# Performance work log

Measured on AMD Instinct MI355X. Metric: run time of the kernel, lower is better.

Reference implementation:

```python
import jax, jax.numpy as jnp
import numpy as np


def setup_inputs() -> dict:
    key = jax.random.key(0)
    ks = jax.random.split(key, 11)
    B, E, R, D = 2048, 20000, 500, 256
    inp = {
        "h": jax.random.uniform(ks[0], (B, E), dtype=jnp.float32),
        "t": jax.random.uniform(ks[1], (B, E), dtype=jnp.float32),
        "r": jax.random.uniform(ks[2], (B, R), dtype=jnp.float32),
        "W_er": jax.random.normal(ks[3], (D, E), dtype=jnp.float32) * 0.02,
        "W_ei": jax.random.normal(ks[4], (D, E), dtype=jnp.float32) * 0.02,
        "W_ej": jax.random.normal(ks[5], (D, E), dtype=jnp.float32) * 0.02,
        "W_ek": jax.random.normal(ks[6], (D, E), dtype=jnp.float32) * 0.02,
        "W_rr": jax.random.normal(ks[7], (D, R), dtype=jnp.float32) * 0.02,
        "W_ri": jax.random.normal(ks[8], (D, R), dtype=jnp.float32) * 0.02,
        "W_rj": jax.random.normal(ks[9], (D, R), dtype=jnp.float32) * 0.02,
        "W_rk": jax.random.normal(ks[10], (D, R), dtype=jnp.float32) * 0.02,
    }
    return inp


def reference(h, t, r, W_er, W_ei, W_ej, W_ek, W_rr, W_ri, W_rj, W_rk):
    # entity / relation projections (nn.Linear, no bias): x @ W^T -> [B, D]
    H_r, H_i, H_j, H_k = h @ W_er.T, h @ W_ei.T, h @ W_ej.T, h @ W_ek.T
    T_r, T_i, T_j, T_k = t @ W_er.T, t @ W_ei.T, t @ W_ej.T, t @ W_ek.T
    R_r, R_i, R_j, R_k = r @ W_rr.T, r @ W_ri.T, r @ W_rj.T, r @ W_rk.T

    # hypercomplex norm per row: sqrt(|R_r|^2 + |R_i|^2 + |R_j|^2 + |R_k|^2) -> [B,1]
    norm = jnp.sqrt(
        jnp.sum(R_r * R_r + R_i * R_i + R_j * R_j + R_k * R_k, axis=1, keepdims=True)
    )
    R_r, R_i, R_j, R_k = norm * R_r, norm * R_i, norm * R_j, norm * R_k

    # Hamilton product H (x) R
    Q_r = H_r * R_r - H_i * R_i - H_j * R_j - H_k * R_k
    Q_i = H_r * R_i + H_i * R_r + H_j * R_k - H_k * R_j
    Q_j = H_r * R_j - H_i * R_k + H_j * R_r + H_k * R_i
    Q_k = H_r * R_k + H_i * R_j - H_j * R_i + H_k * R_r

    # diag(Q @ T^T) == rowwise dot sum(Q*T, axis=1) -- O(B*d) form of the anti-pattern
    score = jnp.sum(Q_r * T_r + Q_i * T_i + Q_j * T_j + Q_k * T_k, axis=1, keepdims=True)
    return jax.nn.sigmoid(score)
```

## Files before the change

kernel.cpp:

```cpp
#include <hip/hip_runtime.h>


using bf16x8 = __attribute__((ext_vector_type(8))) short;
using f32x4  = __attribute__((ext_vector_type(4))) float;
using f32x16 = __attribute__((ext_vector_type(16))) float;

#define DEVINL static __device__ __forceinline__

DEVINL void split2(float x0, float x1, unsigned& h, unsigned& l) {
  unsigned u0 = __float_as_uint(x0), u1 = __float_as_uint(x1);
  unsigned h0 = u0 & 0xFFFF0000u, h1 = u1 & 0xFFFF0000u;
  h = (u0 >> 16) | h1;
  float r0 = x0 - __uint_as_float(h0);
  float r1 = x1 - __uint_as_float(h1);
  l = (__float_as_uint(r0) >> 16) | (__float_as_uint(r1) & 0xFFFF0000u);
}

DEVINL void gload16(const void* g, void* l) {
  __builtin_amdgcn_global_load_lds(
      (const __attribute__((address_space(1))) unsigned*)g,
      (__attribute__((address_space(3))) unsigned*)l, 16, 0, 0);
}

__global__ void convert_img(const float* __restrict__ src0,
                            const float* __restrict__ src1, int rows0,
                            int srcK, char* __restrict__ dst, int ktiles)
{
  const int kt = blockIdx.x, rt = blockIdx.y;
  const int m  = threadIdx.x;
  const int row = rt * 256 + m;
  const float* srow = (row < rows0) ? (src0 + (size_t)row * srcK)
                                    : (src1 + (size_t)(row - rows0) * srcK);
  char* base = dst + ((size_t)rt * ktiles + kt) * 32768
             + (m >> 5) * 2048 + (m & 31) * 16;
#pragma unroll
  for (int oct = 0; oct < 4; ++oct) {
    int k0 = kt * 32 + oct * 8;
    float x[8];
    if (k0 + 8 <= srcK) {
      float4 v0 = *(const float4*)(srow + k0);
      float4 v1 = *(const float4*)(srow + k0 + 4);
      x[0] = v0.x; x[1] = v0.y; x[2] = v0.z; x[3] = v0.w;
      x[4] = v1.x; x[5] = v1.y; x[6] = v1.z; x[7] = v1.w;
    } else {
#pragma unroll
      for (int j = 0; j < 8; ++j) x[j] = (k0 + j < srcK) ? srow[k0 + j] : 0.f;
    }
    unsigned hh[4], ll[4];
    split2(x[0], x[1], hh[0], ll[0]);
    split2(x[2], x[3], hh[1], ll[1]);
    split2(x[4], x[5], hh[2], ll[2]);
    split2(x[6], x[7], hh[3], ll[3]);
    int off = (oct >> 1) * 1024 + (oct & 1) * 512;
    *(uint4*)(base + off)         = make_uint4(hh[0], hh[1], hh[2], hh[3]);
    *(uint4*)(base + 16384 + off) = make_uint4(ll[0], ll[1], ll[2], ll[3]);
  }
}

__global__ __launch_bounds__(512, 2) void gemm_img(
    const char* __restrict__ Aimg, const char* __restrict__ Bimg, int ktiles,
    float* __restrict__ C, int MT, int NT, int KS, int swz)
{
  __shared__ __align__(16) char smem[131072];
  const int tid = threadIdx.x;
  const int bid = blockIdx.x;

  int mt, nt, ks;
  if (swz) {
    int x = bid & 7, w = bid >> 3;
    nt = w & 3;
    int g = x + (w >> 2) * 8;
    mt = g & 15; ks = g >> 4;
  } else {
    nt = bid % NT; int q = bid / NT; mt = q % MT; ks = q / MT;
  }

  const int kt0 = (ktiles * ks) / KS;
  const int kt1 = (ktiles * (ks + 1)) / KS;

  const char* Ab = Aimg + ((size_t)mt * ktiles + kt0) * 32768;
  const char* Bb = Bimg + ((size_t)nt * ktiles + kt0) * 32768;

  const int wid = tid >> 6, lane = tid & 63;
  const int wr = wid >> 2, wc = wid & 3;

  f32x16 acc[4][2];
#pragma unroll
  for (int mb = 0; mb < 4; ++mb)
#pragma unroll
    for (int nb = 0; nb < 2; ++nb)
#pragma unroll
      for (int e = 0; e < 16; ++e) acc[mb][nb][e] = 0.f;

  {
    const char* As = Ab + wid * 4096 + lane * 16;
    const char* Bs = Bb + wid * 4096 + lane * 16;
#pragma unroll
    for (int i = 0; i < 4; ++i) gload16(As + i * 1024, smem + wid * 4096 + i * 1024);
#pragma unroll
    for (int i = 0; i < 4; ++i) gload16(Bs + i * 1024, smem + 32768 + wid * 4096 + i * 1024);
  }
  asm volatile("s_waitcnt vmcnt(0)" ::: "memory");
  __builtin_amdgcn_s_barrier();

  for (int kt = kt0; kt < kt1; ++kt) {
    char* bufc = smem + (size_t)((kt - kt0) & 1) * 65536;
    char* bufn = smem + (size_t)(((kt - kt0) & 1) ^ 1) * 65536;
    const bool nx = (kt + 1 < kt1);

    if (nx) {
      const char* As = Ab + (size_t)(kt + 1 - kt0) * 32768 + wid * 4096 + lane * 16;
      const char* Bs = Bb + (size_t)(kt + 1 - kt0) * 32768 + wid * 4096 + lane * 16;
#pragma unroll
      for (int i = 0; i < 4; ++i) gload16(As + i * 1024, bufn + wid * 4096 + i * 1024);
#pragma unroll
      for (int i = 0; i < 4; ++i) gload16(Bs + i * 1024, bufn + 32768 + wid * 4096 + i * 1024);
    }

    bf16x8 bh[2][2], bl[2][2];
#pragma unroll
    for (int nb = 0; nb < 2; ++nb)
#pragma unroll
      for (int s = 0; s < 2; ++s) {
        const char* p = bufc + 32768 + (wc * 2 + nb) * 2048 + s * 1024 + lane * 16;
        bh[nb][s] = *(const bf16x8*)p;
        bl[nb][s] = *(const bf16x8*)(p + 16384);
      }

    __builtin_amdgcn_s_setprio(1);
#pragma unroll
    for (int mb = 0; mb < 4; ++mb) {
      const char* p = bufc + (wr * 4 + mb) * 2048 + lane * 16;
      bf16x8 ah0 = *(const bf16x8*)(p);
      bf16x8 al0 = *(const bf16x8*)(p + 16384);
      bf16x8 ah1 = *(const bf16x8*)(p + 1024);
      bf16x8 al1 = *(const bf16x8*)(p + 1024 + 16384);
#pragma unroll
      for (int nb = 0; nb < 2; ++nb) {
        f32x16* a = &acc[mb][nb];
        *a = __builtin_amdgcn_mfma_f32_32x32x16_bf16(ah0, bh[nb][0], *a, 0, 0, 0);
        *a = __builtin_amdgcn_mfma_f32_32x32x16_bf16(al0, bh[nb][0], *a, 0, 0, 0);
        *a = __builtin_amdgcn_mfma_f32_32x32x16_bf16(ah0, bl[nb][0], *a, 0, 0, 0);
        *a = __builtin_amdgcn_mfma_f32_32x32x16_bf16(ah1, bh[nb][1], *a, 0, 0, 0);
        *a = __builtin_amdgcn_mfma_f32_32x32x16_bf16(al1, bh[nb][1], *a, 0, 0, 0);
        *a = __builtin_amdgcn_mfma_f32_32x32x16_bf16(ah1, bl[nb][1], *a, 0, 0, 0);
      }
    }
    __builtin_amdgcn_s_setprio(0);

    asm volatile("s_waitcnt vmcnt(0)" ::: "memory");
    __builtin_amdgcn_s_barrier();
  }

  float* Cb = C + (size_t)ks * (size_t)(MT * 256) * 1024;
  const long rowbase = (long)mt * 256 + wr * 128 + 4 * (lane >> 5);
  const long colbase = (long)nt * 256 + wc * 64 + (lane & 31);
#pragma unroll
  for (int mb = 0; mb < 4; ++mb)
#pragma unroll
    for (int nb = 0; nb < 2; ++nb)
#pragma unroll
      for (int reg = 0; reg < 16; ++reg) {
        long row = rowbase + mb * 32 + (reg & 3) + 8 * (reg >> 2);
        long col = colbase + nb * 32;
        Cb[(size_t)row * 1024 + col] = acc[mb][nb][reg];
      }
}

__global__ void convert_b16(const float* __restrict__ src, int srcK,
                            char* __restrict__ dst)
{
  const int tile = blockIdx.x;
  const int wrow = threadIdx.x;
  char* base = dst + (size_t)tile * 32768;
  const float* srow = src + (size_t)wrow * srcK;
#pragma unroll
  for (int kc8 = 0; kc8 < 4; ++kc8) {
    int k0 = tile * 32 + kc8 * 8;
    float x[8];
    if (k0 + 8 <= srcK) {
      float4 v0 = *(const float4*)(srow + k0);
      float4 v1 = *(const float4*)(srow + k0 + 4);
      x[0] = v0.x; x[1] = v0.y; x[2] = v0.z; x[3] = v0.w;
      x[4] = v1.x; x[5] = v1.y; x[6] = v1.z; x[7] = v1.w;
    } else {
#pragma unroll
      for (int j = 0; j < 8; ++j) x[j] = (k0 + j < srcK) ? srow[k0 + j] : 0.f;
    }
    unsigned hh[4], ll[4];
    split2(x[0], x[1], hh[0], ll[0]);
    split2(x[2], x[3], hh[1], ll[1]);
    split2(x[4], x[5], hh[2], ll[2]);
    split2(x[6], x[7], hh[3], ll[3]);
    int lchunk = (wrow & 15) + kc8 * 16;
    int n16 = wrow >> 4;
    *(uint4*)(base + (size_t)n16 * 1024 + lchunk * 16)         = make_uint4(hh[0], hh[1], hh[2], hh[3]);
    *(uint4*)(base + 16384 + (size_t)n16 * 1024 + lchunk * 16) = make_uint4(ll[0], ll[1], ll[2], ll[3]);
  }
}

__global__ void pad_r(const float* __restrict__ src, float* __restrict__ dst)
{
  int row = blockIdx.y;
  int k = threadIdx.x * 4;
  float4 v = make_float4(0.f, 0.f, 0.f, 0.f);
  if (k + 3 < 500) v = *(const float4*)(src + (size_t)row * 500 + k);
  *(float4*)(dst + (size_t)row * 512 + k) = v;
}

__global__ __launch_bounds__(512, 2) void gemm3p(
    const float* __restrict__ A0, const float* __restrict__ A1, int mtA0, long lda,
    const char* __restrict__ Bimg, int ktilesTot,
    float* __restrict__ C, long ldc, int MT, int NT, int KS, int swz)
{
  extern __shared__ char smemd[];
  const int tid = threadIdx.x;
  const int bid = blockIdx.x;

  int mt, nt, ks;
  if (swz) {
    int x = bid & 7, w = bid >> 3;
    nt = w & 3;
    int g = x + (w >> 2) * 8;
    mt = g & 15; ks = g >> 4;
  } else {
    nt = bid % NT; int q = bid / NT; mt = q % MT; ks = q / MT;
  }

  const int kt0 = (ktilesTot * ks) / KS;
  const int kt1 = (ktilesTot * (ks + 1)) / KS;

  const float* Ablk = (mt < mtA0) ? (A0 + (size_t)mt * 256 * lda)
                                  : (A1 + (size_t)(mt - mtA0) * 256 * lda);
  const char* Bt = Bimg + ((size_t)nt * ktilesTot + kt0) * 32768;

  const int wid = tid >> 6, lane = tid & 63;
  const int wr = wid >> 2, wc = wid & 3;
  const int l15 = lane & 15, lq = lane >> 4;

  const float* aSrc = Ablk + (size_t)(wid * 32 + (lane >> 3)) * lda
                      + (size_t)kt0 * 32 + 4 * (lane & 7);

  int awoff[4];
  {
    int kg = (lane & 7) >> 1, half = lane & 1;
#pragma unroll
    for (int i = 0; i < 4; ++i) {
      int m15 = (lane >> 3) + 8 * (i & 1);
      awoff[i] = (2 * wid + (i >> 1)) * 2048 + (((m15 ^ kg) + kg * 16) << 4) + half * 8;
    }
  }
  const int aroff = (((l15 ^ lq) + lq * 16) << 4);
  const int bbase = 32768 + (wc * 4) * 1024 + lane * 16;

  f32x4 acc[8][4];
#pragma unroll
  for (int m = 0; m < 8; ++m)
#pragma unroll
    for (int j = 0; j < 4; ++j)
#pragma unroll
      for (int e = 0; e < 4; ++e) acc[m][j][e] = 0.f;

  float4 aR[4];

#define ISSUE_A(KT)                                                            \
  {                                                                            \
    const float* p_ = aSrc + (size_t)((KT) - kt0) * 32;                        \
    _Pragma("unroll")                                                          \
    for (int i = 0; i < 4; ++i) aR[i] = *(const float4*)(p_ + (size_t)(8 * i) * lda); \
  }
#define ISSUE_B(DST, KT)                                                       \
  {                                                                            \
    const char* p_ = Bt + (size_t)((KT) - kt0) * 32768 + wid * 4096 + lane * 16; \
    _Pragma("unroll")                                                          \
    for (int i = 0; i < 4; ++i)                                                \
      gload16(p_ + i * 1024, (DST) + 32768 + wid * 4096 + i * 1024);           \
  }
#define WRITE_A(DST)                                                           \
  {                                                                            \
    _Pragma("unroll")                                                          \
    for (int i = 0; i < 4; ++i) {                                              \
      unsigned h0_, l0_, h1_, l1_;                                             \
      split2(aR[i].x, aR[i].y, h0_, l0_);                                      \
      split2(aR[i].z, aR[i].w, h1_, l1_);                                      \
      *(uint2*)((DST) + awoff[i])        = make_uint2(h0_, h1_);               \
      *(uint2*)((DST) + awoff[i] + 1024) = make_uint2(l0_, l1_);               \
    }                                                                          \
  }

  ISSUE_A(kt0);
  ISSUE_B(smemd, kt0);
  WRITE_A(smemd);
  asm volatile("s_waitcnt vmcnt(0)" ::: "memory");
  asm volatile("s_waitcnt lgkmcnt(0)" ::: "memory");
  __builtin_amdgcn_s_barrier();

  for (int kt = kt0; kt < kt1; ++kt) {
    char* bufc = smemd + (size_t)((kt - kt0) & 1) * 65536;
    char* bufn = smemd + (size_t)(((kt - kt0) & 1) ^ 1) * 65536;
    const bool nx = (kt + 1 < kt1);

    if (nx) { ISSUE_A(kt + 1); ISSUE_B(bufn, kt + 1); }

    bf16x8 bh[4], bl[4];
#pragma unroll
    for (int j = 0; j < 4; ++j) {
      bh[j] = *(const bf16x8*)(bufc + bbase + j * 1024);
      bl[j] = *(const bf16x8*)(bufc + bbase + j * 1024 + 16384);
    }

    __builtin_amdgcn_s_setprio(1);
#pragma unroll
    for (int m = 0; m < 4; ++m) {
      const char* ab = bufc + (wr * 8 + m) * 2048;
      bf16x8 ah = *(const bf16x8*)(ab + aroff);
      bf16x8 al = *(const bf16x8*)(ab + aroff + 1024);
#pragma unroll
      for (int j = 0; j < 4; ++j) {
        acc[m][j] = __builtin_amdgcn_mfma_f32_16x16x32_bf16(ah, bh[j], acc[m][j], 0, 0, 0);
        acc[m][j] = __builtin_amdgcn_mfma_f32_16x16x32_bf16(al, bh[j], acc[m][j], 0, 0, 0);
        acc[m][j] = __builtin_amdgcn_mfma_f32_16x16x32_bf16(ah, bl[j], acc[m][j], 0, 0, 0);
      }
    }
    __builtin_amdgcn_s_setprio(0);

    __builtin_amdgcn_sched_barrier(0);
    if (nx) WRITE_A(bufn);

    __builtin_amdgcn_s_setprio(1);
#pragma unroll
    for (int m = 4; m < 8; ++m) {
      const char* ab = bufc + (wr * 8 + m) * 2048;
      bf16x8 ah = *(const bf16x8*)(ab + aroff);
      bf16x8 al = *(const bf16x8*)(ab + aroff + 1024);
#pragma unroll
      for (int j = 0; j < 4; ++j) {
        acc[m][j] = __builtin_amdgcn_mfma_f32_16x16x32_bf16(ah, bh[j], acc[m][j], 0, 0, 0);
        acc[m][j] = __builtin_amdgcn_mfma_f32_16x16x32_bf16(al, bh[j], acc[m][j], 0, 0, 0);
        acc[m][j] = __builtin_amdgcn_mfma_f32_16x16x32_bf16(ah, bl[j], acc[m][j], 0, 0, 0);
      }
    }
    __builtin_amdgcn_s_setprio(0);

    asm volatile("s_waitcnt vmcnt(0)" ::: "memory");
    asm volatile("s_waitcnt lgkmcnt(0)" ::: "memory");
    __builtin_amdgcn_s_barrier();
  }
#undef ISSUE_A
#undef ISSUE_B
#undef WRITE_A

  float* Cb = C + (size_t)ks * (size_t)(MT * 256) * (size_t)ldc;
  const long rowbase = (long)mt * 256 + wr * 128 + lq * 4;
  const long colbase = (long)nt * 256 + wc * 64 + l15;
#pragma unroll
  for (int m = 0; m < 8; ++m)
#pragma unroll
    for (int j = 0; j < 4; ++j)
#pragma unroll
      for (int reg = 0; reg < 4; ++reg) {
        long row = rowbase + m * 16 + reg;
        long col = colbase + j * 16;
        Cb[(size_t)row * ldc + col] = acc[m][j][reg];
      }
}

__global__ void epilogue_kernel(const float* __restrict__ C1, const float* __restrict__ C2,
                                float* __restrict__ out, int KS)
{
  const int b = blockIdx.x;
  const int d = threadIdx.x;
  const size_t SZ = 4096ull * 1024ull;

  float Hq[4], Tq[4], Rq[4];
#pragma unroll
  for (int q = 0; q < 4; ++q) {
    float hv = 0.f, tv = 0.f;
    for (int ks = 0; ks < KS; ++ks) {
      hv += C1[ks * SZ + (size_t)b * 1024 + q * 256 + d];
      tv += C1[ks * SZ + (size_t)(b + 2048) * 1024 + q * 256 + d];
    }
    Hq[q] = hv; Tq[q] = tv;
    Rq[q] = C2[(size_t)b * 1024 + q * 256 + d];
  }
  float nn = Rq[0]*Rq[0] + Rq[1]*Rq[1] + Rq[2]*Rq[2] + Rq[3]*Rq[3];
  float Qr = Hq[0]*Rq[0] - Hq[1]*Rq[1] - Hq[2]*Rq[2] - Hq[3]*Rq[3];
  float Qi = Hq[0]*Rq[1] + Hq[1]*Rq[0] + Hq[2]*Rq[3] - Hq[3]*Rq[2];
  float Qj = Hq[0]*Rq[2] - Hq[1]*Rq[3] + Hq[2]*Rq[0] + Hq[3]*Rq[1];
  float Qk = Hq[0]*Rq[3] + Hq[1]*Rq[2] - Hq[2]*Rq[1] + Hq[3]*Rq[0];
  float ss = Qr*Tq[0] + Qi*Tq[1] + Qj*Tq[2] + Qk*Tq[3];

#pragma unroll
  for (int o = 32; o; o >>= 1) {
    ss += __shfl_xor(ss, o);
    nn += __shfl_xor(nn, o);
  }
  __shared__ float red[8];
  int lane = d & 63, w = d >> 6;
  if (lane == 0) { red[w] = ss; red[4 + w] = nn; }
  __syncthreads();
  if (d == 0) {
    float S = red[0] + red[1] + red[2] + red[3];
    float N = red[4] + red[5] + red[6] + red[7];
    float score = sqrtf(N) * S;
    out[b] = 1.f / (1.f + expf(-score));
  }
}

extern "C" void kernel_launch(void* const* d_in, const int* in_sizes, int n_in,
                              void* d_out, int out_size, void* d_ws, size_t ws_size,
                              hipStream_t stream)
{
  const float* h = (const float*)d_in[0];
  const float* t = (const float*)d_in[1];
  const float* r = (const float*)d_in[2];
  const float* We[4] = {(const float*)d_in[3], (const float*)d_in[4],
                        (const float*)d_in[5], (const float*)d_in[6]};
  const float* Wr[4] = {(const float*)d_in[7], (const float*)d_in[8],
                        (const float*)d_in[9], (const float*)d_in[10]};
  float* out = (float*)d_out;
  char* ws = (char*)d_ws;

  const size_t offA  = 0;
  const size_t offB  = 327680000;
  const size_t offWr = offB + 81920000;
  const size_t offRi = offWr + 2097152;
  const size_t offC1 = offRi + 4194304;
  const size_t C1sz  = 4096ull * 1024ull * 4ull;
  const size_t offC2 = offC1 + 4 * C1sz;
  const size_t needImg = offC2 + 8388608;

  if (ws_size >= needImg) {
    float* C1 = (float*)(ws + offC1);
    float* C2 = (float*)(ws + offC2);

    convert_img<<<dim3(625, 16), 256, 0, stream>>>(h, t, 2048, 20000, ws + offA, 625);
    for (int q = 0; q < 4; ++q) {
      convert_img<<<dim3(625, 1), 256, 0, stream>>>(
          We[q], We[q], 2048, 20000, ws + offB + (size_t)q * 625 * 32768, 625);
      convert_img<<<dim3(16, 1), 256, 0, stream>>>(
          Wr[q], Wr[q], 2048, 500, ws + offWr + (size_t)q * 16 * 32768, 16);
    }
    convert_img<<<dim3(16, 8), 256, 0, stream>>>(r, r, 4096, 500, ws + offRi, 16);

    gemm_img<<<dim3(256), 512, 0, stream>>>(
        ws + offA, ws + offB, 625, C1, 16, 4, 4, 1);
    gemm_img<<<dim3(32), 512, 0, stream>>>(
        ws + offRi, ws + offWr, 16, C2, 8, 4, 1, 0);

    epilogue_kernel<<<dim3(2048), 256, 0, stream>>>(C1, C2, out, 4);
    return;
  }

  const size_t fB  = 0;
  const size_t fWr = 81920000;
  const size_t fR  = fWr + 2097152;
  const size_t fC1 = fR + 4194304;
  const int KS = (ws_size >= fC1 + 4 * C1sz + 8388608ull) ? 4 : 2;
  const size_t fC2 = fC1 + (size_t)KS * C1sz;

  float* rpad = (float*)(ws + fR);
  float* C1   = (float*)(ws + fC1);
  float* C2   = (float*)(ws + fC2);

  for (int q = 0; q < 4; ++q) {
    convert_b16<<<dim3(625), 256, 0, stream>>>(We[q], 20000, ws + fB + (size_t)q * 625 * 32768);
    convert_b16<<<dim3(16), 256, 0, stream>>>(Wr[q], 500, ws + fWr + (size_t)q * 16 * 32768);
  }
  pad_r<<<dim3(1, 2048), 128, 0, stream>>>(r, rpad);

  gemm3p<<<dim3(16 * 4 * KS), 512, 131072, stream>>>(
      h, t, 8, 20000L, (const char*)(ws + fB), 625,
      C1, 1024L, 16, 4, KS, KS == 4 ? 1 : 0);
  gemm3p<<<dim3(32), 512, 131072, stream>>>(
      rpad, rpad, 8, 512L, (const char*)(ws + fWr), 16,
      C2, 1024L, 8, 4, 1, 0);

  epilogue_kernel<<<dim3(2048), 256, 0, stream>>>(C1, C2, out, KS);
}
```

Measured before the change: 690.1 us.

## Coalesce fp32-to-bf16 split conversion via LDS transpose and split-K the relation GEMM

The conversion kernels now read 64-row by 32-column tiles with coalesced float4 loads into shared memory, then split them into hi/lo bf16 images, instead of each thread walking its own row. The four weight conversions are merged into single launches. The small relation GEMM gets split-K across up to 8 slices, with the epilogue summing the partials. Launch bounds on the GEMM change from 2 to 1 blocks per CU. Together these target the bandwidth-bound conversion phase and the under-occupied relation GEMM, at the cost of an extra LDS round trip and more partial-sum traffic.

```diff
diff --git a/kernel.cpp b/kernel.cpp
--- a/kernel.cpp
+++ b/kernel.cpp
@@ -22,47 +22,79 @@
       (__attribute__((address_space(3))) unsigned*)l, 16, 0, 0);
 }
 
-__global__ void convert_img(const float* __restrict__ src0,
-                            const float* __restrict__ src1, int rows0,
-                            int srcK, char* __restrict__ dst, int ktiles)
-{
-  const int kt = blockIdx.x, rt = blockIdx.y;
-  const int m  = threadIdx.x;
-  const int row = rt * 256 + m;
-  const float* srow = (row < rows0) ? (src0 + (size_t)row * srcK)
-                                    : (src1 + (size_t)(row - rows0) * srcK);
-  char* base = dst + ((size_t)rt * ktiles + kt) * 32768
-             + (m >> 5) * 2048 + (m & 31) * 16;
-#pragma unroll
-  for (int oct = 0; oct < 4; ++oct) {
-    int k0 = kt * 32 + oct * 8;
+DEVINL void conv_body(const float* srow, int srcK, int kt, int rb,
+                      char* dst, int ktiles, float ld[64][36], int t)
+{
+  {
+    int r = t >> 2, kc = (t & 3) * 8;
+    int k0 = kt * 32 + kc;
+    const float* s = srow + (size_t)r * srcK;
+    float4 v0, v1;
+    if (k0 + 8 <= srcK) {
+      v0 = *(const float4*)(s + k0);
+      v1 = *(const float4*)(s + k0 + 4);
+    } else {
+      float x[8];
+#pragma unroll
+      for (int j = 0; j < 8; ++j) x[j] = (k0 + j < srcK) ? s[k0 + j] : 0.f;
+      v0 = make_float4(x[0], x[1], x[2], x[3]);
+      v1 = make_float4(x[4], x[5], x[6], x[7]);
+    }
+    *(float4*)&ld[r][kc]     = v0;
+    *(float4*)&ld[r][kc + 4] = v1;
+  }
+  __syncthreads();
+  {
+    int g = t >> 7, s = (t >> 6) & 1, kh = (t >> 5) & 1, r31 = t & 31;
+    int row = g * 32 + r31;
+    int k = s * 16 + kh * 8;
     float x[8];
-    if (k0 + 8 <= srcK) {
-      float4 v0 = *(const float4*)(srow + k0);
-      float4 v1 = *(const float4*)(srow + k0 + 4);
-      x[0] = v0.x; x[1] = v0.y; x[2] = v0.z; x[3] = v0.w;
-      x[4] = v1.x; x[5] = v1.y; x[6] = v1.z; x[7] = v1.w;
-    } else {
-#pragma unroll
-      for (int j = 0; j < 8; ++j) x[j] = (k0 + j < srcK) ? srow[k0 + j] : 0.f;
-    }
-    unsigned hh[4], ll[4];
-    split2(x[0], x[1], hh[0], ll[0]);
-    split2(x[2], x[3], hh[1], ll[1]);
-    split2(x[4], x[5], hh[2], ll[2]);
-    split2(x[6], x[7], hh[3], ll[3]);
-    int off = (oct >> 1) * 1024 + (oct & 1) * 512;
-    *(uint4*)(base + off)         = make_uint4(hh[0], hh[1], hh[2], hh[3]);
-    *(uint4*)(base + 16384 + off) = make_uint4(ll[0], ll[1], ll[2], ll[3]);
-  }
-}
-
-__global__ __launch_bounds__(512, 2) void gemm_img(
+#pragma unroll
+    for (int j = 0; j < 8; ++j) x[j] = ld[row][k + j];
+    unsigned hh[4], llv[4];
+    split2(x[0], x[1], hh[0], llv[0]);
+    split2(x[2], x[3], hh[1], llv[1]);
+    split2(x[4], x[5], hh[2], llv[2]);
+    split2(x[6], x[7], hh[3], llv[3]);
+    int tile_rt = rb >> 2;
+    int gbase = (rb & 3) * 2;
+    char* base = dst + ((size_t)tile_rt * ktiles + kt) * 32768
+               + (gbase + g) * 2048 + s * 1024 + kh * 512 + r31 * 16;
+    *(uint4*)base           = make_uint4(hh[0], hh[1], hh[2], hh[3]);
+    *(uint4*)(base + 16384) = make_uint4(llv[0], llv[1], llv[2], llv[3]);
+  }
+}
+
+__global__ void convert_img2(const float* __restrict__ src0,
+                             const float* __restrict__ src1, int rows0,
+                             int srcK, char* __restrict__ dst, int ktiles)
+{
+  __shared__ float ld[64][36];
+  const int kt = blockIdx.x, rb = blockIdx.y, t = threadIdx.x;
+  int row0 = rb * 64;
+  const float* srow = (row0 < rows0) ? (src0 + (size_t)row0 * srcK)
+                                     : (src1 + (size_t)(row0 - rows0) * srcK);
+  conv_body(srow, srcK, kt, rb, dst, ktiles, ld, t);
+}
+
+__global__ void convert_q4(const float* __restrict__ p0, const float* __restrict__ p1,
+                           const float* __restrict__ p2, const float* __restrict__ p3,
+                           int rbPerQ, int srcK, char* __restrict__ dst,
+                           size_t qStride, int ktiles)
+{
+  __shared__ float ld[64][36];
+  const int kt = blockIdx.x, t = threadIdx.x;
+  const int q = blockIdx.y / rbPerQ, rb = blockIdx.y % rbPerQ;
+  const float* src = (q == 0) ? p0 : (q == 1) ? p1 : (q == 2) ? p2 : p3;
+  conv_body(src + (size_t)(rb * 64) * srcK, srcK, kt, rb,
+            dst + (size_t)q * qStride, ktiles, ld, t);
+}
+
+__global__ __launch_bounds__(512, 1) void gemm_img(
     const char* __restrict__ Aimg, const char* __restrict__ Bimg, int ktiles,
     float* __restrict__ C, int MT, int NT, int KS, int swz)
 {
   __shared__ __align__(16) char smem[131072];
-  const int tid = threadIdx.x;
   const int bid = blockIdx.x;
 
   int mt, nt, ks;
@@ -81,7 +113,7 @@
   const char* Ab = Aimg + ((size_t)mt * ktiles + kt0) * 32768;
   const char* Bb = Bimg + ((size_t)nt * ktiles + kt0) * 32768;
 
-  const int wid = tid >> 6, lane = tid & 63;
+  const int wid = threadIdx.x >> 6, lane = threadIdx.x & 63;
   const int wr = wid >> 2, wc = wid & 3;
 
   f32x16 acc[4][2];
@@ -366,22 +398,24 @@
 }
 
 __global__ void epilogue_kernel(const float* __restrict__ C1, const float* __restrict__ C2,
-                                float* __restrict__ out, int KS)
+                                float* __restrict__ out, int KS1, int KS2)
 {
   const int b = blockIdx.x;
   const int d = threadIdx.x;
-  const size_t SZ = 4096ull * 1024ull;
+  const size_t SZ1 = 4096ull * 1024ull;
+  const size_t SZ2 = 2048ull * 1024ull;
 
   float Hq[4], Tq[4], Rq[4];
 #pragma unroll
   for (int q = 0; q < 4; ++q) {
-    float hv = 0.f, tv = 0.f;
-    for (int ks = 0; ks < KS; ++ks) {
-      hv += C1[ks * SZ + (size_t)b * 1024 + q * 256 + d];
-      tv += C1[ks * SZ + (size_t)(b + 2048) * 1024 + q * 256 + d];
-    }
-    Hq[q] = hv; Tq[q] = tv;
-    Rq[q] = C2[(size_t)b * 1024 + q * 256 + d];
+    float hv = 0.f, tv = 0.f, rv = 0.f;
+    for (int ks = 0; ks < KS1; ++ks) {
+      hv += C1[ks * SZ1 + (size_t)b * 1024 + q * 256 + d];
+      tv += C1[ks * SZ1 + (size_t)(b + 2048) * 1024 + q * 256 + d];
+    }
+    for (int ks = 0; ks < KS2; ++ks)
+      rv += C2[ks * SZ2 + (size_t)b * 1024 + q * 256 + d];
+    Hq[q] = hv; Tq[q] = tv; Rq[q] = rv;
   }
   float nn = Rq[0]*Rq[0] + Rq[1]*Rq[1] + Rq[2]*Rq[2] + Rq[3]*Rq[3];
   float Qr = Hq[0]*Rq[0] - Hq[1]*Rq[1] - Hq[2]*Rq[2] - Hq[3]*Rq[3];
@@ -427,28 +461,31 @@
   const size_t offRi = offWr + 2097152;
   const size_t offC1 = offRi + 4194304;
   const size_t C1sz  = 4096ull * 1024ull * 4ull;
+  const size_t C2sz  = 2048ull * 1024ull * 4ull;
   const size_t offC2 = offC1 + 4 * C1sz;
-  const size_t needImg = offC2 + 8388608;
+  const size_t needImg = offC2 + C2sz;
 
   if (ws_size >= needImg) {
     float* C1 = (float*)(ws + offC1);
     float* C2 = (float*)(ws + offC2);
 
-    convert_img<<<dim3(625, 16), 256, 0, stream>>>(h, t, 2048, 20000, ws + offA, 625);
-    for (int q = 0; q < 4; ++q) {
-      convert_img<<<dim3(625, 1), 256, 0, stream>>>(
-          We[q], We[q], 2048, 20000, ws + offB + (size_t)q * 625 * 32768, 625);
-      convert_img<<<dim3(16, 1), 256, 0, stream>>>(
-          Wr[q], Wr[q], 2048, 500, ws + offWr + (size_t)q * 16 * 32768, 16);
-    }
-    convert_img<<<dim3(16, 8), 256, 0, stream>>>(r, r, 4096, 500, ws + offRi, 16);
+    int KS2 = (int)((ws_size - offC2) / C2sz);
+    if (KS2 > 8) KS2 = 8;
+    if (KS2 < 1) KS2 = 1;
+
+    convert_img2<<<dim3(625, 64), 256, 0, stream>>>(h, t, 2048, 20000, ws + offA, 625);
+    convert_q4<<<dim3(625, 16), 256, 0, stream>>>(
+        We[0], We[1], We[2], We[3], 4, 20000, ws + offB, (size_t)625 * 32768, 625);
+    convert_q4<<<dim3(16, 16), 256, 0, stream>>>(
+        Wr[0], Wr[1], Wr[2], Wr[3], 4, 500, ws + offWr, (size_t)16 * 32768, 16);
+    convert_img2<<<dim3(16, 32), 256, 0, stream>>>(r, r, 2048, 500, ws + offRi, 16);
 
     gemm_img<<<dim3(256), 512, 0, stream>>>(
         ws + offA, ws + offB, 625, C1, 16, 4, 4, 1);
-    gemm_img<<<dim3(32), 512, 0, stream>>>(
-        ws + offRi, ws + offWr, 16, C2, 8, 4, 1, 0);
-
-    epilogue_kernel<<<dim3(2048), 256, 0, stream>>>(C1, C2, out, 4);
+    gemm_img<<<dim3(8 * 4 * KS2), 512, 0, stream>>>(
+        ws + offRi, ws + offWr, 16, C2, 8, 4, KS2, 0);
+
+    epilogue_kernel<<<dim3(2048), 256, 0, stream>>>(C1, C2, out, 4, KS2);
     return;
   }
 
@@ -476,5 +513,5 @@
       rpad, rpad, 8, 512L, (const char*)(ws + fWr), 16,
       C2, 1024L, 8, 4, 1, 0);
 
-  epilogue_kernel<<<dim3(2048), 256, 0, stream>>>(C1, C2, out, KS);
-}
+  epilogue_kernel<<<dim3(2048), 256, 0, stream>>>(C1, C2, out, KS, 1);
+}
```

Result: faster. 593.2 us (-14.0%).
